# Kernel optimization log

Hardware: AMD Instinct MI355X
Metric: run time of the kernel (lower is better)

## Reference

```python
import jax, jax.numpy as jnp
import numpy as np
import math

B, N, L, ED, H = 2, 32, 4, 64, 4   # graphs, nodes/graph, layers, embed_dim, heads
HD = ED // H
EPS = 1e-5


def _ln(x, g, b):
    m = x.mean(-1, keepdims=True)
    v = ((x - m) ** 2).mean(-1, keepdims=True)
    return (x - m) * jax.lax.rsqrt(v + EPS) * g + b


def _layer(x, W, b, lg, lb, fW, fb, fg, fbeta):
    # NOTE: in the torch source, ModuleList([Linear]*4) shares ONE linear for
    # q/k/v1/v2 and ONE LayerNorm for norms[0..2]; we reproduce that sharing.
    h = (x @ W.T + b).reshape(B, N, N, H, HD)
    q = _ln(h, lg, lb)                                    # q == k (shared LN)
    scores = jnp.einsum('bxahd,bayhd->bxayh', q, q) / math.sqrt(HD)
    att = jax.nn.softmax(scores, axis=2)                  # softmax over 'a'
    xu = jnp.einsum('bxahd,bayhd->bxayhd', h, h)          # v1 == v2 == h
    xu = _ln(xu, lg, lb)                                  # shared LN again
    xu = jnp.einsum('bxayh,bxayhd->bxyhd', att, xu).reshape(B, N, N, ED)
    y = jnp.concatenate([x, xu], axis=-1) @ fW.T + fb
    return _ln(y, fg, fbeta)


def _diag_offdiag_maxpool(x):
    # x: (B, ED, N, N)
    diag = jnp.diagonal(x, axis1=-2, axis2=-1)            # (B, ED, N)
    max_diag = diag.max(axis=2)                           # (B, ED)
    val = jnp.abs(max_diag.max() + (-x).max())
    eye = jnp.eye(N, dtype=x.dtype)
    max_offdiag = (x - val * eye).max(axis=(2, 3))        # (B, ED)
    return jnp.concatenate([max_diag, max_offdiag], axis=1)  # (B, 2*ED)


def setup_inputs() -> dict:
    key = jax.random.key(0)
    ks = jax.random.split(key, 12)
    E = 1024
    g = jax.random.randint(ks[0], (E,), 0, B)
    ls = jax.random.randint(ks[1], (E,), 0, N)
    ld = jax.random.randint(ks[2], (E,), 0, N)
    edge_index = jnp.stack([g * N + ls, g * N + ld]).astype(jnp.int64)
    batch = (jnp.arange(B * N) // N).astype(jnp.int64)
    std = 0.02
    return {
        'edge_index': edge_index,
        'batch': batch,
        'W0': jax.random.normal(ks[3], (ED, 1), jnp.float32) * std,
        'b0': jnp.zeros((ED,), jnp.float32),
        'Ws': jax.random.normal(ks[4], (L - 1, ED, ED), jnp.float32) * std,
        'bs': jnp.zeros((L - 1, ED), jnp.float32),
        'ln_g': jnp.ones((L, HD), jnp.float32),
        'ln_b': jnp.zeros((L, HD), jnp.float32),
        'fW0': jax.random.normal(ks[5], (ED, 1 + ED), jnp.float32) * std,
        'fb0': jnp.zeros((ED,), jnp.float32),
        'fWs': jax.random.normal(ks[6], (L - 1, ED, 2 * ED), jnp.float32) * std,
        'fbs': jnp.zeros((L - 1, ED), jnp.float32),
        'fln_g': jnp.ones((L, ED), jnp.float32),
        'fln_b': jnp.zeros((L, ED), jnp.float32),
        'opW': jax.random.normal(ks[7], (L, ED // 2, 2 * ED), jnp.float32) * std,
        'opb': jnp.zeros((L, ED // 2), jnp.float32),
    }


def reference(edge_index, batch, W0, b0, Ws, bs, ln_g, ln_b,
              fW0, fb0, fWs, fbs, fln_g, fln_b, opW, opb):
    # to_dense_adj with edge_attr = 1.0
    g = batch[edge_index[0]]
    ls = edge_index[0] - g * N
    ld = edge_index[1] - g * N
    adj = jnp.zeros((B, N, N), jnp.float32).at[g, ls, ld].add(1.0)
    idx = jnp.arange(N)
    adj = adj.at[:, idx, idx].set(2.0)
    x = adj[..., None]                                    # (B, N, N, 1)

    scores = jnp.zeros((B, ED // 2), jnp.float32)
    for i in range(L):
        W = W0 if i == 0 else Ws[i - 1]
        b = b0 if i == 0 else bs[i - 1]
        fW = fW0 if i == 0 else fWs[i - 1]
        fb = fb0 if i == 0 else fbs[i - 1]
        x = _layer(x, W, b, ln_g[i], ln_b[i], fW, fb, fln_g[i], fln_b[i])
        pooled = _diag_offdiag_maxpool(jnp.transpose(x, (0, 3, 1, 2)))
        scores = scores + pooled @ opW[i].T + opb[i]

    # BatchNorm1d(momentum=1.0, affine=False), training mode -> batch stats
    m = scores.mean(axis=0)
    v = scores.var(axis=0)
    return (scores - m) / jnp.sqrt(v + EPS)
```

## Files before the change

### kernel.cpp

```cpp
#include <hip/hip_runtime.h>
#include <math.h>

#define EPS 1e-5f

#define AG_LOAD(p)     __hip_atomic_load((p), __ATOMIC_RELAXED, __HIP_MEMORY_SCOPE_AGENT)
#define AG_STORE(p, v) __hip_atomic_store((p), (v), __ATOMIC_RELAXED, __HIP_MEMORY_SCOPE_AGENT)

struct Params {
    const int* ei; const int* batch; int E;
    const float* W0; const float* b0; const float* Ws; const float* bs;
    const float* ln_g; const float* ln_b;
    const float* fW0; const float* fb0; const float* fWs; const float* fbs;
    const float* fln_g; const float* fln_b;
    const float* opW; const float* opb;
    float* hA; float* qA;
    float* hB; float* qB;
    float* xbuf;
    float* Pmin; float* Poff; float* Pdg;
    int* bar;
    float* out;
};

__launch_bounds__(512, 1)
__global__ void k0(Params p) {
    const int tid  = threadIdx.x;
    const int blk  = blockIdx.x;
    const int gtid = blk * 512 + tid;
    const int c    = gtid & 63;
    const int d    = c & 15;
    const int rl   = tid >> 6;
    const int row  = gtid >> 6;
    const int y    = row & 31;
    const int r0     = blk * 8;
    const int b_blk  = r0 >> 10;
    const int xi_blk = (r0 >> 5) & 31;
    const int y0     = r0 & 31;
    const int rld    = xi_blk - y0;

    __shared__ float xslab[32];
    __shared__ float yslab[256];
    __shared__ float xu_s[8][64];
    __shared__ float xrow[8][64];

    if (blk == 0 && tid == 0) p.bar[0] = 0;

    if (tid < 32)  xslab[tid] = 0.0f;
    if (tid < 256) yslab[tid] = 0.0f;
    __syncthreads();
    for (int e2 = tid; e2 < p.E; e2 += 512) {
        int e0 = p.ei[e2], e1 = p.ei[p.E + e2];
        int g  = p.batch[e0];
        if (g == b_blk) {
            int ls = e0 - g * 32, ld = e1 - g * 32;
            if (ls == xi_blk) atomicAdd(&xslab[ld], 1.0f);
            unsigned dy = (unsigned)(ld - y0);
            if (dy < 8u) atomicAdd(&yslab[ls * 8 + dy], 1.0f);
        }
    }
    __syncthreads();
    if (tid == 0) xslab[xi_blk] = 2.0f;
    if (tid < 8)  yslab[(y0 + tid) * 8 + tid] = 2.0f;
    __syncthreads();

    {
        const float gl = p.ln_g[d], bl = p.ln_b[d];
        float Wc = p.W0[c], bc = p.b0[c];
        float sW = Wc, sB = bc;
        #pragma unroll
        for (int m = 1; m < 16; m <<= 1) {
            sW += __shfl_xor(sW, m, 16);
            sB += __shfl_xor(sB, m, 16);
        }
        float Ac = Wc - sW * 0.0625f;
        float Bc = bc - sB * 0.0625f;
        float sAA = Ac * Ac, sAB = Ac * Bc, sBB = Bc * Bc;
        #pragma unroll
        for (int m = 1; m < 16; m <<= 1) {
            sAA += __shfl_xor(sAA, m, 16);
            sAB += __shfl_xor(sAB, m, 16);
            sBB += __shfl_xor(sBB, m, 16);
        }
        const float varW = sAA * 0.0625f, covWB = sAB * 0.0625f, varB = sBB * 0.0625f;
        const float adjv = xslab[y];

        float sarr[32], narr[32];
        #pragma unroll
        for (int a = 0; a < 32; ++a) {
            float vx = xslab[a];
            float vy = yslab[a * 8 + rl];
            float hx = fmaf(Wc, vx, bc);
            float hy = fmaf(Wc, vy, bc);
            float qx = fmaf(Ac, vx, Bc) *
                       rsqrtf(fmaf(fmaf(varW, vx, 2.0f * covWB), vx, varB) + EPS) * gl + bl;
            float qy = fmaf(Ac, vy, Bc) *
                       rsqrtf(fmaf(fmaf(varW, vy, 2.0f * covWB), vy, varB) + EPS) * gl + bl;
            float rdot = qx * qy;
            float pp   = hx * hy;
            float rsum = pp, rsq = pp * pp;
            #pragma unroll
            for (int m = 1; m < 16; m <<= 1) {
                rdot += __shfl_xor(rdot, m, 16);
                rsum += __shfl_xor(rsum, m, 16);
                rsq  += __shfl_xor(rsq,  m, 16);
            }
            sarr[a] = rdot * 0.25f;
            float pmean = rsum * 0.0625f;
            float pvar  = fmaxf(rsq * 0.0625f - pmean * pmean, 0.0f);
            narr[a] = (pp - pmean) * rsqrtf(pvar + EPS) * gl;
        }
        float mx = sarr[0];
        #pragma unroll
        for (int a = 1; a < 32; ++a) mx = fmaxf(mx, sarr[a]);
        float lsum = 0.0f, asum = 0.0f;
        #pragma unroll
        for (int a = 0; a < 32; ++a) {
            float ee = __expf(sarr[a] - mx);
            lsum += ee;
            asum = fmaf(ee, narr[a], asum);
        }
        xu_s[rl][c] = asum / lsum + bl;

        const float* Wr2 = p.fW0 + c * 65;
        float acc2 = fmaf(Wr2[0], adjv, p.fb0[c]);
        #pragma unroll
        for (int j = 0; j < 64; ++j) acc2 = fmaf(Wr2[1 + j], xu_s[rl][j], acc2);
        float t1 = acc2;
        #pragma unroll
        for (int m = 1; m < 64; m <<= 1) t1 += __shfl_xor(t1, m, 64);
        float mu = t1 * (1.0f / 64.0f);
        float dv2 = acc2 - mu;
        float t2 = dv2 * dv2;
        #pragma unroll
        for (int m = 1; m < 64; m <<= 1) t2 += __shfl_xor(t2, m, 64);
        float xnew = dv2 * rsqrtf(t2 * (1.0f / 64.0f) + EPS) * p.fln_g[c] + p.fln_b[c];
        xrow[rl][c]  = xnew;
        p.xbuf[gtid] = xnew;
    }
    __syncthreads();

    if (tid < 64) {
        float mn = 1e30f, off = -1e30f, dg = -1e30f;
        #pragma unroll
        for (int r2 = 0; r2 < 8; ++r2) {
            float v = xrow[r2][tid];
            mn = fminf(mn, v);
            if (r2 == rld) dg = v; else off = fmaxf(off, v);
        }
        int o = blk * 64 + tid;
        p.Pmin[o] = mn; p.Poff[o] = off; p.Pdg[o] = dg;
    }

    {
        const float* Wr = p.Ws + c * 64;
        float acc = p.bs[c];
        #pragma unroll
        for (int j = 0; j < 64; ++j) acc = fmaf(Wr[j], xrow[rl][j], acc);
        p.hA[gtid] = acc;
        float s1 = acc;
        #pragma unroll
        for (int m = 1; m < 16; m <<= 1) s1 += __shfl_xor(s1, m, 16);
        float mean = s1 * 0.0625f;
        float dv = acc - mean;
        float s2 = dv * dv;
        #pragma unroll
        for (int m = 1; m < 16; m <<= 1) s2 += __shfl_xor(s2, m, 16);
        p.qA[gtid] = dv * rsqrtf(s2 * 0.0625f + EPS) * p.ln_g[16 + d] + p.ln_b[16 + d];
    }
}

__launch_bounds__(512, 1)
__global__ void klayer(Params p, int layer, int is_last) {
    const int tid  = threadIdx.x;
    const int blk  = blockIdx.x;
    const int gtid = blk * 512 + tid;
    const int c    = gtid & 63;
    const int d    = c & 15;
    const int rl   = tid >> 6;
    const int row  = gtid >> 6;
    const int y    = row & 31;
    const int b    = row >> 10;
    const int r0     = blk * 8;
    const int b_blk  = r0 >> 10;
    const int xi_blk = (r0 >> 5) & 31;
    const int y0     = r0 & 31;
    const int rld    = xi_blk - y0;
    const int slab_off = (b_blk * 1024 + xi_blk * 32) * 64;

    const float* hin = (layer == 2) ? p.hB : p.hA;
    const float* qin = (layer == 2) ? p.qB : p.qA;
    float* hout = (layer == 1) ? p.hB : p.hA;
    float* qout = (layer == 1) ? p.qB : p.qA;

    __shared__ float qx_s[2048], hx_s[2048];
    __shared__ float xrow[8][64], xu_s[8][64];
    __shared__ float sm_mn[512], sm_off[512], sm_dg[512];
    __shared__ float psum[512];
    __shared__ float vals[4];
    __shared__ float scores_s[64];
    __shared__ int tailflag;

    float xv = p.xbuf[gtid];
    float4 qsl = ((const float4*)(qin + slab_off))[tid];
    float4 hsl = ((const float4*)(hin + slab_off))[tid];
    const float* qy = qin + (b * 1024 + y) * 64 + c;
    const float* hy = hin + (b * 1024 + y) * 64 + c;
    float qyv[32], hyv[32];
    #pragma unroll
    for (int a = 0; a < 32; ++a) {
        qyv[a] = qy[a * 2048];
        hyv[a] = hy[a * 2048];
    }
    xrow[rl][c] = xv;
    ((float4*)qx_s)[tid] = qsl;
    ((float4*)hx_s)[tid] = hsl;
    __syncthreads();

    const float gl = p.ln_g[layer * 16 + d], bl = p.ln_b[layer * 16 + d];
    float sarr[32], narr[32];
    #pragma unroll
    for (int a = 0; a < 32; ++a) {
        float qxv = qx_s[a * 64 + c];
        float hxv = hx_s[a * 64 + c];
        float rdot = qxv * qyv[a];
        float pp   = hxv * hyv[a];
        float rsum = pp, rsq = pp * pp;
        #pragma unroll
        for (int m = 1; m < 16; m <<= 1) {
            rdot += __shfl_xor(rdot, m, 16);
            rsum += __shfl_xor(rsum, m, 16);
            rsq  += __shfl_xor(rsq,  m, 16);
        }
        sarr[a] = rdot * 0.25f;
        float pmean = rsum * 0.0625f;
        float pvar  = fmaxf(rsq * 0.0625f - pmean * pmean, 0.0f);
        narr[a] = (pp - pmean) * rsqrtf(pvar + EPS) * gl;
    }
    float mx = sarr[0];
    #pragma unroll
    for (int a = 1; a < 32; ++a) mx = fmaxf(mx, sarr[a]);
    float lsum = 0.0f, asum = 0.0f;
    #pragma unroll
    for (int a = 0; a < 32; ++a) {
        float ee = __expf(sarr[a] - mx);
        lsum += ee;
        asum = fmaf(ee, narr[a], asum);
    }
    xu_s[rl][c] = asum / lsum + bl;

    const float* Wr2 = p.fWs + (layer - 1) * 8192 + c * 128;
    float acc2 = p.fbs[(layer - 1) * 64 + c];
    #pragma unroll
    for (int j = 0; j < 64; ++j) acc2 = fmaf(Wr2[j], xrow[rl][j], acc2);
    #pragma unroll
    for (int j = 0; j < 64; ++j) acc2 = fmaf(Wr2[64 + j], xu_s[rl][j], acc2);
    float t1 = acc2;
    #pragma unroll
    for (int m = 1; m < 64; m <<= 1) t1 += __shfl_xor(t1, m, 64);
    float mu = t1 * (1.0f / 64.0f);
    float dv2 = acc2 - mu;
    float t2 = dv2 * dv2;
    #pragma unroll
    for (int m = 1; m < 64; m <<= 1) t2 += __shfl_xor(t2, m, 64);
    float xnew = dv2 * rsqrtf(t2 * (1.0f / 64.0f) + EPS) *
                 p.fln_g[layer * 64 + c] + p.fln_b[layer * 64 + c];
    __syncthreads();
    xrow[rl][c] = xnew;
    if (!is_last) p.xbuf[gtid] = xnew;
    __syncthreads();

    if (tid < 64) {
        float mn = 1e30f, off = -1e30f, dg = -1e30f;
        #pragma unroll
        for (int r2 = 0; r2 < 8; ++r2) {
            float v = xrow[r2][tid];
            mn = fminf(mn, v);
            if (r2 == rld) dg = v; else off = fmaxf(off, v);
        }
        int o = layer * 16384 + blk * 64 + tid;
        if (is_last) {
            AG_STORE(&p.Pmin[o], mn); AG_STORE(&p.Poff[o], off); AG_STORE(&p.Pdg[o], dg);
        } else {
            p.Pmin[o] = mn; p.Poff[o] = off; p.Pdg[o] = dg;
        }
    }

    if (!is_last) {
        const float* Wr = p.Ws + layer * 4096 + c * 64;
        float acc = p.bs[layer * 64 + c];
        #pragma unroll
        for (int j = 0; j < 64; ++j) acc = fmaf(Wr[j], xrow[rl][j], acc);
        hout[gtid] = acc;
        float s1 = acc;
        #pragma unroll
        for (int m = 1; m < 16; m <<= 1) s1 += __shfl_xor(s1, m, 16);
        float mean = s1 * 0.0625f;
        float dv = acc - mean;
        float s2 = dv * dv;
        #pragma unroll
        for (int m = 1; m < 16; m <<= 1) s2 += __shfl_xor(s2, m, 16);
        qout[gtid] = dv * rsqrtf(s2 * 0.0625f + EPS) *
                     p.ln_g[(layer + 1) * 16 + d] + p.ln_b[(layer + 1) * 16 + d];
        return;
    }

    __syncthreads();
    if (tid == 0) {
        int r = __hip_atomic_fetch_add(p.bar, 1, __ATOMIC_RELAXED,
                                       __HIP_MEMORY_SCOPE_AGENT);
        tailflag = (r == 255) ? 1 : 0;
    }
    __syncthreads();
    if (!tailflag) return;

    {
        int l = tid >> 7, bb = (tid >> 6) & 1, e = tid & 63;
        float mn = 1e30f, off = -1e30f, dg = -1e30f;
        for (int k = 0; k < 128; ++k) {
            int o = l * 16384 + (bb * 128 + k) * 64 + e;
            float vmn, voff, vdg;
            if (l == 3) { vmn = AG_LOAD(&p.Pmin[o]); voff = AG_LOAD(&p.Poff[o]); vdg = AG_LOAD(&p.Pdg[o]); }
            else        { vmn = p.Pmin[o];           voff = p.Poff[o];           vdg = p.Pdg[o]; }
            mn  = fminf(mn,  vmn);
            off = fmaxf(off, voff);
            dg  = fmaxf(dg,  vdg);
        }
        sm_mn[tid] = mn; sm_off[tid] = off; sm_dg[tid] = dg;
    }
    __syncthreads();
    if (tid < 4) {
        float gmx = -1e30f, gmn = 1e30f;
        for (int i2 = 0; i2 < 128; ++i2) {
            gmx = fmaxf(gmx, sm_dg[tid * 128 + i2]);
            gmn = fminf(gmn, sm_mn[tid * 128 + i2]);
        }
        vals[tid] = fabsf(gmx - gmn);
    }
    __syncthreads();
    {
        int bb = tid >> 8, cc = (tid >> 3) & 31, pp = tid & 7;
        float a2 = 0.0f;
        for (int l = 0; l < 4; ++l) {
            float val = vals[l];
            const float* Wr = p.opW + l * 4096 + cc * 128;
            int base = l * 128 + bb * 64;
            for (int j = pp * 16; j < pp * 16 + 16; ++j) {
                float pv;
                if (j < 64) pv = sm_dg[base + j];
                else        pv = fmaxf(sm_off[base + j - 64], sm_dg[base + j - 64] - val);
                a2 = fmaf(Wr[j], pv, a2);
            }
        }
        psum[tid] = a2;
    }
    __syncthreads();
    if (tid < 64) {
        int bb = tid >> 5, cc = tid & 31;
        float a2 = 0.0f;
        for (int l = 0; l < 4; ++l) a2 += p.opb[l * 32 + cc];
        for (int pp = 0; pp < 8; ++pp) a2 += psum[bb * 256 + cc * 8 + pp];
        scores_s[tid] = a2;
    }
    __syncthreads();
    if (tid < 32) {
        float sA = scores_s[tid], sB = scores_s[32 + tid];
        float mu2 = 0.5f * (sA + sB);
        float va = 0.5f * ((sA - mu2) * (sA - mu2) + (sB - mu2) * (sB - mu2));
        float inv = rsqrtf(va + EPS);
        p.out[tid]      = (sA - mu2) * inv;
        p.out[32 + tid] = (sB - mu2) * inv;
    }
}

extern "C" void kernel_launch(void* const* d_in, const int* in_sizes, int n_in,
                              void* d_out, int out_size, void* d_ws, size_t ws_size,
                              hipStream_t stream) {
    Params prm;
    prm.ei    = (const int*)d_in[0];
    prm.batch = (const int*)d_in[1];
    prm.E     = in_sizes[0] / 2;
    prm.W0    = (const float*)d_in[2];
    prm.b0    = (const float*)d_in[3];
    prm.Ws    = (const float*)d_in[4];
    prm.bs    = (const float*)d_in[5];
    prm.ln_g  = (const float*)d_in[6];
    prm.ln_b  = (const float*)d_in[7];
    prm.fW0   = (const float*)d_in[8];
    prm.fb0   = (const float*)d_in[9];
    prm.fWs   = (const float*)d_in[10];
    prm.fbs   = (const float*)d_in[11];
    prm.fln_g = (const float*)d_in[12];
    prm.fln_b = (const float*)d_in[13];
    prm.opW   = (const float*)d_in[14];
    prm.opb   = (const float*)d_in[15];

    float* ws = (float*)d_ws;
    prm.hA    = ws;
    prm.qA    = prm.hA   + 131072;
    prm.hB    = prm.qA   + 131072;
    prm.qB    = prm.hB   + 131072;
    prm.xbuf  = prm.qB   + 131072;
    prm.Pmin  = prm.xbuf + 131072;
    prm.Poff  = prm.Pmin + 65536;
    prm.Pdg   = prm.Poff + 65536;
    prm.bar   = (int*)(prm.Pdg + 65536);
    prm.out   = (float*)d_out;

    k0<<<256, 512, 0, stream>>>(prm);
    klayer<<<256, 512, 0, stream>>>(prm, 1, 0);
    klayer<<<256, 512, 0, stream>>>(prm, 2, 0);
    klayer<<<256, 512, 0, stream>>>(prm, 3, 1);
}
```

Measured before the change: 196.7 us.

## Use online softmax and chunked y-loads to cut register pressure in layer kernels

```diff
diff --git a/kernel.cpp b/kernel.cpp
--- a/kernel.cpp
+++ b/kernel.cpp
@@ -39,14 +39,15 @@
 
     __shared__ float xslab[32];
     __shared__ float yslab[256];
-    __shared__ float xu_s[8][64];
-    __shared__ float xrow[8][64];
+    __shared__ float xu[512];
+    __shared__ float xrow[512];
 
     if (blk == 0 && tid == 0) p.bar[0] = 0;
 
     if (tid < 32)  xslab[tid] = 0.0f;
     if (tid < 256) yslab[tid] = 0.0f;
     __syncthreads();
+    #pragma unroll 1
     for (int e2 = tid; e2 < p.E; e2 += 512) {
         int e0 = p.ei[e2], e1 = p.ei[p.E + e2];
         int g  = p.batch[e0];
@@ -62,87 +63,84 @@
     if (tid < 8)  yslab[(y0 + tid) * 8 + tid] = 2.0f;
     __syncthreads();
 
+    const float gl = p.ln_g[d], bl = p.ln_b[d];
+    float Wc = p.W0[c], bc = p.b0[c];
+    float sW = Wc, sB = bc;
+    #pragma unroll
+    for (int m = 1; m < 16; m <<= 1) {
+        sW += __shfl_xor(sW, m, 16);
+        sB += __shfl_xor(sB, m, 16);
+    }
+    float Ac = Wc - sW * 0.0625f;
+    float Bc = bc - sB * 0.0625f;
+    float sAA = Ac * Ac, sAB = Ac * Bc, sBB = Bc * Bc;
+    #pragma unroll
+    for (int m = 1; m < 16; m <<= 1) {
+        sAA += __shfl_xor(sAA, m, 16);
+        sAB += __shfl_xor(sAB, m, 16);
+        sBB += __shfl_xor(sBB, m, 16);
+    }
+    const float varW = sAA * 0.0625f, covWB = sAB * 0.0625f, varB = sBB * 0.0625f;
+    const float adjv = xslab[y];
+
+    float mrun = -1e30f, lrun = 0.0f, arun = 0.0f;
+    #pragma unroll 1
+    for (int a = 0; a < 32; ++a) {
+        float vx = xslab[a];
+        float vy = yslab[a * 8 + rl];
+        float hx = fmaf(Wc, vx, bc);
+        float hy = fmaf(Wc, vy, bc);
+        float qx = fmaf(Ac, vx, Bc) *
+                   rsqrtf(fmaf(fmaf(varW, vx, 2.0f * covWB), vx, varB) + EPS) * gl + bl;
+        float qy = fmaf(Ac, vy, Bc) *
+                   rsqrtf(fmaf(fmaf(varW, vy, 2.0f * covWB), vy, varB) + EPS) * gl + bl;
+        float rdot = qx * qy;
+        float pp   = hx * hy;
+        float rsum = pp, rsq = pp * pp;
+        #pragma unroll
+        for (int m = 1; m < 16; m <<= 1) {
+            rdot += __shfl_xor(rdot, m, 16);
+            rsum += __shfl_xor(rsum, m, 16);
+            rsq  += __shfl_xor(rsq,  m, 16);
+        }
+        float s     = rdot * 0.25f;
+        float pmean = rsum * 0.0625f;
+        float pvar  = fmaxf(rsq * 0.0625f - pmean * pmean, 0.0f);
+        float nrm   = (pp - pmean) * rsqrtf(pvar + EPS) * gl;
+        float nm  = fmaxf(mrun, s);
+        float scl = __expf(mrun - nm);
+        float e   = __expf(s - nm);
+        lrun = lrun * scl + e;
+        arun = arun * scl + e * nrm;
+        mrun = nm;
+    }
+    xu[tid] = arun / lrun + bl;
+
+    const float* Wr2 = p.fW0 + c * 65;
+    float acc2 = fmaf(Wr2[0], adjv, p.fb0[c]);
     {
-        const float gl = p.ln_g[d], bl = p.ln_b[d];
-        float Wc = p.W0[c], bc = p.b0[c];
-        float sW = Wc, sB = bc;
-        #pragma unroll
-        for (int m = 1; m < 16; m <<= 1) {
-            sW += __shfl_xor(sW, m, 16);
-            sB += __shfl_xor(sB, m, 16);
-        }
-        float Ac = Wc - sW * 0.0625f;
-        float Bc = bc - sB * 0.0625f;
-        float sAA = Ac * Ac, sAB = Ac * Bc, sBB = Bc * Bc;
-        #pragma unroll
-        for (int m = 1; m < 16; m <<= 1) {
-            sAA += __shfl_xor(sAA, m, 16);
-            sAB += __shfl_xor(sAB, m, 16);
-            sBB += __shfl_xor(sBB, m, 16);
-        }
-        const float varW = sAA * 0.0625f, covWB = sAB * 0.0625f, varB = sBB * 0.0625f;
-        const float adjv = xslab[y];
-
-        float sarr[32], narr[32];
-        #pragma unroll
-        for (int a = 0; a < 32; ++a) {
-            float vx = xslab[a];
-            float vy = yslab[a * 8 + rl];
-            float hx = fmaf(Wc, vx, bc);
-            float hy = fmaf(Wc, vy, bc);
-            float qx = fmaf(Ac, vx, Bc) *
-                       rsqrtf(fmaf(fmaf(varW, vx, 2.0f * covWB), vx, varB) + EPS) * gl + bl;
-            float qy = fmaf(Ac, vy, Bc) *
-                       rsqrtf(fmaf(fmaf(varW, vy, 2.0f * covWB), vy, varB) + EPS) * gl + bl;
-            float rdot = qx * qy;
-            float pp   = hx * hy;
-            float rsum = pp, rsq = pp * pp;
-            #pragma unroll
-            for (int m = 1; m < 16; m <<= 1) {
-                rdot += __shfl_xor(rdot, m, 16);
-                rsum += __shfl_xor(rsum, m, 16);
-                rsq  += __shfl_xor(rsq,  m, 16);
-            }
-            sarr[a] = rdot * 0.25f;
-            float pmean = rsum * 0.0625f;
-            float pvar  = fmaxf(rsq * 0.0625f - pmean * pmean, 0.0f);
-            narr[a] = (pp - pmean) * rsqrtf(pvar + EPS) * gl;
-        }
-        float mx = sarr[0];
-        #pragma unroll
-        for (int a = 1; a < 32; ++a) mx = fmaxf(mx, sarr[a]);
-        float lsum = 0.0f, asum = 0.0f;
-        #pragma unroll
-        for (int a = 0; a < 32; ++a) {
-            float ee = __expf(sarr[a] - mx);
-            lsum += ee;
-            asum = fmaf(ee, narr[a], asum);
-        }
-        xu_s[rl][c] = asum / lsum + bl;
-
-        const float* Wr2 = p.fW0 + c * 65;
-        float acc2 = fmaf(Wr2[0], adjv, p.fb0[c]);
-        #pragma unroll
-        for (int j = 0; j < 64; ++j) acc2 = fmaf(Wr2[1 + j], xu_s[rl][j], acc2);
-        float t1 = acc2;
-        #pragma unroll
-        for (int m = 1; m < 64; m <<= 1) t1 += __shfl_xor(t1, m, 64);
-        float mu = t1 * (1.0f / 64.0f);
-        float dv2 = acc2 - mu;
-        float t2 = dv2 * dv2;
-        #pragma unroll
-        for (int m = 1; m < 64; m <<= 1) t2 += __shfl_xor(t2, m, 64);
-        float xnew = dv2 * rsqrtf(t2 * (1.0f / 64.0f) + EPS) * p.fln_g[c] + p.fln_b[c];
-        xrow[rl][c]  = xnew;
-        p.xbuf[gtid] = xnew;
-    }
+        const float* xw = xu + rl * 64;
+        #pragma unroll 8
+        for (int j = 0; j < 64; ++j) acc2 = fmaf(Wr2[1 + j], xw[j], acc2);
+    }
+    float t1 = acc2;
+    #pragma unroll
+    for (int m = 1; m < 64; m <<= 1) t1 += __shfl_xor(t1, m, 64);
+    float mu = t1 * (1.0f / 64.0f);
+    float dv2 = acc2 - mu;
+    float t2 = dv2 * dv2;
+    #pragma unroll
+    for (int m = 1; m < 64; m <<= 1) t2 += __shfl_xor(t2, m, 64);
+    float xnew = dv2 * rsqrtf(t2 * (1.0f / 64.0f) + EPS) * p.fln_g[c] + p.fln_b[c];
+    xrow[tid]    = xnew;
+    p.xbuf[gtid] = xnew;
     __syncthreads();
 
     if (tid < 64) {
         float mn = 1e30f, off = -1e30f, dg = -1e30f;
         #pragma unroll
         for (int r2 = 0; r2 < 8; ++r2) {
-            float v = xrow[r2][tid];
+            float v = xrow[r2 * 64 + tid];
             mn = fminf(mn, v);
             if (r2 == rld) dg = v; else off = fmaxf(off, v);
         }
@@ -151,10 +149,14 @@
     }
 
     {
-        const float* Wr = p.Ws + c * 64;
+        const float4* W4 = (const float4*)(p.Ws + c * 64);
+        const float4* X4 = (const float4*)(xrow + rl * 64);
         float acc = p.bs[c];
-        #pragma unroll
-        for (int j = 0; j < 64; ++j) acc = fmaf(Wr[j], xrow[rl][j], acc);
+        #pragma unroll 4
+        for (int j = 0; j < 16; ++j) {
+            float4 w = W4[j], x = X4[j];
+            acc += w.x * x.x + w.y * x.y + w.z * x.z + w.w * x.w;
+        }
         p.hA[gtid] = acc;
         float s1 = acc;
         #pragma unroll
@@ -192,7 +194,7 @@
     float* qout = (layer == 1) ? p.qB : p.qA;
 
     __shared__ float qx_s[2048], hx_s[2048];
-    __shared__ float xrow[8][64], xu_s[8][64];
+    __shared__ float xrow[512], xu[512];
     __shared__ float sm_mn[512], sm_off[512], sm_dg[512];
     __shared__ float psum[512];
     __shared__ float vals[4];
@@ -200,59 +202,71 @@
     __shared__ int tailflag;
 
     float xv = p.xbuf[gtid];
-    float4 qsl = ((const float4*)(qin + slab_off))[tid];
-    float4 hsl = ((const float4*)(hin + slab_off))[tid];
+    float4 qs = ((const float4*)(qin + slab_off))[tid];
+    float4 hs = ((const float4*)(hin + slab_off))[tid];
+    xrow[tid] = xv;
+    ((float4*)qx_s)[tid] = qs;
+    ((float4*)hx_s)[tid] = hs;
+    __syncthreads();
+
+    const float gl = p.ln_g[layer * 16 + d], bl = p.ln_b[layer * 16 + d];
     const float* qy = qin + (b * 1024 + y) * 64 + c;
     const float* hy = hin + (b * 1024 + y) * 64 + c;
-    float qyv[32], hyv[32];
-    #pragma unroll
-    for (int a = 0; a < 32; ++a) {
-        qyv[a] = qy[a * 2048];
-        hyv[a] = hy[a * 2048];
-    }
-    xrow[rl][c] = xv;
-    ((float4*)qx_s)[tid] = qsl;
-    ((float4*)hx_s)[tid] = hsl;
-    __syncthreads();
-
-    const float gl = p.ln_g[layer * 16 + d], bl = p.ln_b[layer * 16 + d];
-    float sarr[32], narr[32];
-    #pragma unroll
-    for (int a = 0; a < 32; ++a) {
-        float qxv = qx_s[a * 64 + c];
-        float hxv = hx_s[a * 64 + c];
-        float rdot = qxv * qyv[a];
-        float pp   = hxv * hyv[a];
-        float rsum = pp, rsq = pp * pp;
-        #pragma unroll
-        for (int m = 1; m < 16; m <<= 1) {
-            rdot += __shfl_xor(rdot, m, 16);
-            rsum += __shfl_xor(rsum, m, 16);
-            rsq  += __shfl_xor(rsq,  m, 16);
-        }
-        sarr[a] = rdot * 0.25f;
-        float pmean = rsum * 0.0625f;
-        float pvar  = fmaxf(rsq * 0.0625f - pmean * pmean, 0.0f);
-        narr[a] = (pp - pmean) * rsqrtf(pvar + EPS) * gl;
-    }
-    float mx = sarr[0];
-    #pragma unroll
-    for (int a = 1; a < 32; ++a) mx = fmaxf(mx, sarr[a]);
-    float lsum = 0.0f, asum = 0.0f;
-    #pragma unroll
-    for (int a = 0; a < 32; ++a) {
-        float ee = __expf(sarr[a] - mx);
-        lsum += ee;
-        asum = fmaf(ee, narr[a], asum);
-    }
-    xu_s[rl][c] = asum / lsum + bl;
-
-    const float* Wr2 = p.fWs + (layer - 1) * 8192 + c * 128;
+
+    float mrun = -1e30f, lrun = 0.0f, arun = 0.0f;
+    #pragma unroll 1
+    for (int ch = 0; ch < 4; ++ch) {
+        float qv8[8], hv8[8];
+        const float* qpc = qy + ch * 8 * 2048;
+        const float* hpc = hy + ch * 8 * 2048;
+        #pragma unroll
+        for (int k = 0; k < 8; ++k) {
+            qv8[k] = qpc[k * 2048];
+            hv8[k] = hpc[k * 2048];
+        }
+        const float* qxc = qx_s + ch * 8 * 64 + c;
+        const float* hxc = hx_s + ch * 8 * 64 + c;
+        #pragma unroll
+        for (int k = 0; k < 8; ++k) {
+            float rdot = qxc[k * 64] * qv8[k];
+            float pp   = hxc[k * 64] * hv8[k];
+            float rsum = pp, rsq = pp * pp;
+            #pragma unroll
+            for (int m = 1; m < 16; m <<= 1) {
+                rdot += __shfl_xor(rdot, m, 16);
+                rsum += __shfl_xor(rsum, m, 16);
+                rsq  += __shfl_xor(rsq,  m, 16);
+            }
+            float s     = rdot * 0.25f;
+            float pmean = rsum * 0.0625f;
+            float pvar  = fmaxf(rsq * 0.0625f - pmean * pmean, 0.0f);
+            float nrm   = (pp - pmean) * rsqrtf(pvar + EPS) * gl;
+            float nm  = fmaxf(mrun, s);
+            float scl = __expf(mrun - nm);
+            float e   = __expf(s - nm);
+            lrun = lrun * scl + e;
+            arun = arun * scl + e * nrm;
+            mrun = nm;
+        }
+    }
+    xu[tid] = arun / lrun + bl;
+
     float acc2 = p.fbs[(layer - 1) * 64 + c];
-    #pragma unroll
-    for (int j = 0; j < 64; ++j) acc2 = fmaf(Wr2[j], xrow[rl][j], acc2);
-    #pragma unroll
-    for (int j = 0; j < 64; ++j) acc2 = fmaf(Wr2[64 + j], xu_s[rl][j], acc2);
+    {
+        const float4* W4 = (const float4*)(p.fWs + (layer - 1) * 8192 + c * 128);
+        const float4* Xa = (const float4*)(xrow + rl * 64);
+        const float4* Xb = (const float4*)(xu + rl * 64);
+        #pragma unroll 4
+        for (int j = 0; j < 16; ++j) {
+            float4 w = W4[j], x = Xa[j];
+            acc2 += w.x * x.x + w.y * x.y + w.z * x.z + w.w * x.w;
+        }
+        #pragma unroll 4
+        for (int j = 0; j < 16; ++j) {
+            float4 w = W4[16 + j], x = Xb[j];
+            acc2 += w.x * x.x + w.y * x.y + w.z * x.z + w.w * x.w;
+        }
+    }
     float t1 = acc2;
     #pragma unroll
     for (int m = 1; m < 64; m <<= 1) t1 += __shfl_xor(t1, m, 64);
@@ -263,8 +277,7 @@
     for (int m = 1; m < 64; m <<= 1) t2 += __shfl_xor(t2, m, 64);
     float xnew = dv2 * rsqrtf(t2 * (1.0f / 64.0f) + EPS) *
                  p.fln_g[layer * 64 + c] + p.fln_b[layer * 64 + c];
-    __syncthreads();
-    xrow[rl][c] = xnew;
+    xrow[tid] = xnew;
     if (!is_last) p.xbuf[gtid] = xnew;
     __syncthreads();
 
@@ -272,7 +285,7 @@
         float mn = 1e30f, off = -1e30f, dg = -1e30f;
         #pragma unroll
         for (int r2 = 0; r2 < 8; ++r2) {
-            float v = xrow[r2][tid];
+            float v = xrow[r2 * 64 + tid];
             mn = fminf(mn, v);
             if (r2 == rld) dg = v; else off = fmaxf(off, v);
         }
@@ -285,10 +298,14 @@
     }
 
     if (!is_last) {
-        const float* Wr = p.Ws + layer * 4096 + c * 64;
+        const float4* W4 = (const float4*)(p.Ws + layer * 4096 + c * 64);
+        const float4* X4 = (const float4*)(xrow + rl * 64);
         float acc = p.bs[layer * 64 + c];
-        #pragma unroll
-        for (int j = 0; j < 64; ++j) acc = fmaf(Wr[j], xrow[rl][j], acc);
+        #pragma unroll 4
+        for (int j = 0; j < 16; ++j) {
+            float4 w = W4[j], x = X4[j];
+            acc += w.x * x.x + w.y * x.y + w.z * x.z + w.w * x.w;
+        }
         hout[gtid] = acc;
         float s1 = acc;
         #pragma unroll
@@ -303,7 +320,6 @@
         return;
     }
 
-    __syncthreads();
     if (tid == 0) {
         int r = __hip_atomic_fetch_add(p.bar, 1, __ATOMIC_RELAXED,
                                        __HIP_MEMORY_SCOPE_AGENT);
@@ -315,20 +331,30 @@
     {
         int l = tid >> 7, bb = (tid >> 6) & 1, e = tid & 63;
         float mn = 1e30f, off = -1e30f, dg = -1e30f;
-        for (int k = 0; k < 128; ++k) {
-            int o = l * 16384 + (bb * 128 + k) * 64 + e;
-            float vmn, voff, vdg;
-            if (l == 3) { vmn = AG_LOAD(&p.Pmin[o]); voff = AG_LOAD(&p.Poff[o]); vdg = AG_LOAD(&p.Pdg[o]); }
-            else        { vmn = p.Pmin[o];           voff = p.Poff[o];           vdg = p.Pdg[o]; }
-            mn  = fminf(mn,  vmn);
-            off = fmaxf(off, voff);
-            dg  = fmaxf(dg,  vdg);
+        int base = l * 16384 + bb * 128 * 64 + e;
+        if (l == 3) {
+            #pragma unroll 4
+            for (int k = 0; k < 128; ++k) {
+                int o = base + k * 64;
+                mn  = fminf(mn,  AG_LOAD(&p.Pmin[o]));
+                off = fmaxf(off, AG_LOAD(&p.Poff[o]));
+                dg  = fmaxf(dg,  AG_LOAD(&p.Pdg[o]));
+            }
+        } else {
+            #pragma unroll 4
+            for (int k = 0; k < 128; ++k) {
+                int o = base + k * 64;
+                mn  = fminf(mn,  p.Pmin[o]);
+                off = fmaxf(off, p.Poff[o]);
+                dg  = fmaxf(dg,  p.Pdg[o]);
+            }
         }
         sm_mn[tid] = mn; sm_off[tid] = off; sm_dg[tid] = dg;
     }
     __syncthreads();
     if (tid < 4) {
         float gmx = -1e30f, gmn = 1e30f;
+        #pragma unroll 1
         for (int i2 = 0; i2 < 128; ++i2) {
             gmx = fmaxf(gmx, sm_dg[tid * 128 + i2]);
             gmn = fminf(gmn, sm_mn[tid * 128 + i2]);
@@ -339,10 +365,12 @@
     {
         int bb = tid >> 8, cc = (tid >> 3) & 31, pp = tid & 7;
         float a2 = 0.0f;
+        #pragma unroll 1
         for (int l = 0; l < 4; ++l) {
             float val = vals[l];
             const float* Wr = p.opW + l * 4096 + cc * 128;
             int base = l * 128 + bb * 64;
+            #pragma unroll 1
             for (int j = pp * 16; j < pp * 16 + 16; ++j) {
                 float pv;
                 if (j < 64) pv = sm_dg[base + j];
@@ -356,7 +384,9 @@
     if (tid < 64) {
         int bb = tid >> 5, cc = tid & 31;
         float a2 = 0.0f;
+        #pragma unroll
         for (int l = 0; l < 4; ++l) a2 += p.opb[l * 32 + cc];
+        #pragma unroll
         for (int pp = 0; pp < 8; ++pp) a2 += psum[bb * 256 + cc * 8 + pp];
         scores_s[tid] = a2;
     }
```

Result: slower. 203.8 us (+3.7%).

## Split attention reduction across two waves per row with online-softmax merge

Applied to the files above, without the earlier changes.

```diff
diff --git a/kernel.cpp b/kernel.cpp
--- a/kernel.cpp
+++ b/kernel.cpp
@@ -47,6 +47,7 @@
     if (tid < 32)  xslab[tid] = 0.0f;
     if (tid < 256) yslab[tid] = 0.0f;
     __syncthreads();
+    #pragma unroll 1
     for (int e2 = tid; e2 < p.E; e2 += 512) {
         int e0 = p.ei[e2], e1 = p.ei[p.E + e2];
         int g  = p.batch[e0];
@@ -62,80 +63,78 @@
     if (tid < 8)  yslab[(y0 + tid) * 8 + tid] = 2.0f;
     __syncthreads();
 
-    {
-        const float gl = p.ln_g[d], bl = p.ln_b[d];
-        float Wc = p.W0[c], bc = p.b0[c];
-        float sW = Wc, sB = bc;
+    const float gl = p.ln_g[d], bl = p.ln_b[d];
+    float Wc = p.W0[c], bc = p.b0[c];
+    float sW = Wc, sB = bc;
+    #pragma unroll
+    for (int m = 1; m < 16; m <<= 1) {
+        sW += __shfl_xor(sW, m, 16);
+        sB += __shfl_xor(sB, m, 16);
+    }
+    float Ac = Wc - sW * 0.0625f;
+    float Bc = bc - sB * 0.0625f;
+    float sAA = Ac * Ac, sAB = Ac * Bc, sBB = Bc * Bc;
+    #pragma unroll
+    for (int m = 1; m < 16; m <<= 1) {
+        sAA += __shfl_xor(sAA, m, 16);
+        sAB += __shfl_xor(sAB, m, 16);
+        sBB += __shfl_xor(sBB, m, 16);
+    }
+    const float varW = sAA * 0.0625f, covWB = sAB * 0.0625f, varB = sBB * 0.0625f;
+    const float adjv = xslab[y];
+
+    float sarr[32], narr[32];
+    #pragma unroll
+    for (int a = 0; a < 32; ++a) {
+        float vx = xslab[a];
+        float vy = yslab[a * 8 + rl];
+        float hx = fmaf(Wc, vx, bc);
+        float hy = fmaf(Wc, vy, bc);
+        float qx = fmaf(Ac, vx, Bc) *
+                   rsqrtf(fmaf(fmaf(varW, vx, 2.0f * covWB), vx, varB) + EPS) * gl + bl;
+        float qy = fmaf(Ac, vy, Bc) *
+                   rsqrtf(fmaf(fmaf(varW, vy, 2.0f * covWB), vy, varB) + EPS) * gl + bl;
+        float rdot = qx * qy;
+        float pp   = hx * hy;
+        float rsum = pp, rsq = pp * pp;
         #pragma unroll
         for (int m = 1; m < 16; m <<= 1) {
-            sW += __shfl_xor(sW, m, 16);
-            sB += __shfl_xor(sB, m, 16);
-        }
-        float Ac = Wc - sW * 0.0625f;
-        float Bc = bc - sB * 0.0625f;
-        float sAA = Ac * Ac, sAB = Ac * Bc, sBB = Bc * Bc;
-        #pragma unroll
-        for (int m = 1; m < 16; m <<= 1) {
-            sAA += __shfl_xor(sAA, m, 16);
-            sAB += __shfl_xor(sAB, m, 16);
-            sBB += __shfl_xor(sBB, m, 16);
-        }
-        const float varW = sAA * 0.0625f, covWB = sAB * 0.0625f, varB = sBB * 0.0625f;
-        const float adjv = xslab[y];
-
-        float sarr[32], narr[32];
-        #pragma unroll
-        for (int a = 0; a < 32; ++a) {
-            float vx = xslab[a];
-            float vy = yslab[a * 8 + rl];
-            float hx = fmaf(Wc, vx, bc);
-            float hy = fmaf(Wc, vy, bc);
-            float qx = fmaf(Ac, vx, Bc) *
-                       rsqrtf(fmaf(fmaf(varW, vx, 2.0f * covWB), vx, varB) + EPS) * gl + bl;
-            float qy = fmaf(Ac, vy, Bc) *
-                       rsqrtf(fmaf(fmaf(varW, vy, 2.0f * covWB), vy, varB) + EPS) * gl + bl;
-            float rdot = qx * qy;
-            float pp   = hx * hy;
-            float rsum = pp, rsq = pp * pp;
-            #pragma unroll
-            for (int m = 1; m < 16; m <<= 1) {
-                rdot += __shfl_xor(rdot, m, 16);
-                rsum += __shfl_xor(rsum, m, 16);
-                rsq  += __shfl_xor(rsq,  m, 16);
-            }
-            sarr[a] = rdot * 0.25f;
-            float pmean = rsum * 0.0625f;
-            float pvar  = fmaxf(rsq * 0.0625f - pmean * pmean, 0.0f);
-            narr[a] = (pp - pmean) * rsqrtf(pvar + EPS) * gl;
-        }
-        float mx = sarr[0];
-        #pragma unroll
-        for (int a = 1; a < 32; ++a) mx = fmaxf(mx, sarr[a]);
-        float lsum = 0.0f, asum = 0.0f;
-        #pragma unroll
-        for (int a = 0; a < 32; ++a) {
-            float ee = __expf(sarr[a] - mx);
-            lsum += ee;
-            asum = fmaf(ee, narr[a], asum);
-        }
-        xu_s[rl][c] = asum / lsum + bl;
-
-        const float* Wr2 = p.fW0 + c * 65;
-        float acc2 = fmaf(Wr2[0], adjv, p.fb0[c]);
-        #pragma unroll
-        for (int j = 0; j < 64; ++j) acc2 = fmaf(Wr2[1 + j], xu_s[rl][j], acc2);
-        float t1 = acc2;
-        #pragma unroll
-        for (int m = 1; m < 64; m <<= 1) t1 += __shfl_xor(t1, m, 64);
-        float mu = t1 * (1.0f / 64.0f);
-        float dv2 = acc2 - mu;
-        float t2 = dv2 * dv2;
-        #pragma unroll
-        for (int m = 1; m < 64; m <<= 1) t2 += __shfl_xor(t2, m, 64);
-        float xnew = dv2 * rsqrtf(t2 * (1.0f / 64.0f) + EPS) * p.fln_g[c] + p.fln_b[c];
-        xrow[rl][c]  = xnew;
-        p.xbuf[gtid] = xnew;
-    }
+            rdot += __shfl_xor(rdot, m, 16);
+            rsum += __shfl_xor(rsum, m, 16);
+            rsq  += __shfl_xor(rsq,  m, 16);
+        }
+        sarr[a] = rdot * 0.25f;
+        float pmean = rsum * 0.0625f;
+        float pvar  = fmaxf(rsq * 0.0625f - pmean * pmean, 0.0f);
+        narr[a] = (pp - pmean) * rsqrtf(pvar + EPS) * gl;
+    }
+    float mx = sarr[0];
+    #pragma unroll
+    for (int a = 1; a < 32; ++a) mx = fmaxf(mx, sarr[a]);
+    float lsum = 0.0f, asum = 0.0f;
+    #pragma unroll
+    for (int a = 0; a < 32; ++a) {
+        float ee = __expf(sarr[a] - mx);
+        lsum += ee;
+        asum = fmaf(ee, narr[a], asum);
+    }
+    xu_s[rl][c] = asum / lsum + bl;
+
+    const float* Wr2 = p.fW0 + c * 65;
+    float acc2 = fmaf(Wr2[0], adjv, p.fb0[c]);
+    #pragma unroll
+    for (int j = 0; j < 64; ++j) acc2 = fmaf(Wr2[1 + j], xu_s[rl][j], acc2);
+    float t1 = acc2;
+    #pragma unroll
+    for (int m = 1; m < 64; m <<= 1) t1 += __shfl_xor(t1, m, 64);
+    float mu = t1 * (1.0f / 64.0f);
+    float dv2 = acc2 - mu;
+    float t2 = dv2 * dv2;
+    #pragma unroll
+    for (int m = 1; m < 64; m <<= 1) t2 += __shfl_xor(t2, m, 64);
+    float xnew = dv2 * rsqrtf(t2 * (1.0f / 64.0f) + EPS) * p.fln_g[c] + p.fln_b[c];
+    xrow[rl][c]  = xnew;
+    p.xbuf[gtid] = xnew;
     __syncthreads();
 
     if (tid < 64) {
@@ -168,17 +167,19 @@
     }
 }
 
-__launch_bounds__(512, 1)
+__launch_bounds__(1024, 1)
 __global__ void klayer(Params p, int layer, int is_last) {
     const int tid  = threadIdx.x;
     const int blk  = blockIdx.x;
-    const int gtid = blk * 512 + tid;
-    const int c    = gtid & 63;
+    const int rl   = tid >> 7;
+    const int u    = tid & 127;
+    const int w    = u >> 6;
+    const int c    = u & 63;
     const int d    = c & 15;
-    const int rl   = tid >> 6;
-    const int row  = gtid >> 6;
+    const int row  = blk * 8 + rl;
     const int y    = row & 31;
     const int b    = row >> 10;
+    const int ge   = row * 64 + c;
     const int r0     = blk * 8;
     const int b_blk  = r0 >> 10;
     const int xi_blk = (r0 >> 5) & 31;
@@ -192,37 +193,37 @@
     float* qout = (layer == 1) ? p.qB : p.qA;
 
     __shared__ float qx_s[2048], hx_s[2048];
-    __shared__ float xrow[8][64], xu_s[8][64];
+    __shared__ float xrow[512], xu[512];
+    __shared__ float mM[1024], mL[1024], mA[1024];
     __shared__ float sm_mn[512], sm_off[512], sm_dg[512];
     __shared__ float psum[512];
     __shared__ float vals[4];
     __shared__ float scores_s[64];
     __shared__ int tailflag;
 
-    float xv = p.xbuf[gtid];
-    float4 qsl = ((const float4*)(qin + slab_off))[tid];
-    float4 hsl = ((const float4*)(hin + slab_off))[tid];
+    if (w == 0) xrow[rl * 64 + c] = p.xbuf[ge];
+    ((float2*)qx_s)[tid] = ((const float2*)(qin + slab_off))[tid];
+    ((float2*)hx_s)[tid] = ((const float2*)(hin + slab_off))[tid];
     const float* qy = qin + (b * 1024 + y) * 64 + c;
     const float* hy = hin + (b * 1024 + y) * 64 + c;
-    float qyv[32], hyv[32];
-    #pragma unroll
-    for (int a = 0; a < 32; ++a) {
-        qyv[a] = qy[a * 2048];
-        hyv[a] = hy[a * 2048];
-    }
-    xrow[rl][c] = xv;
-    ((float4*)qx_s)[tid] = qsl;
-    ((float4*)hx_s)[tid] = hsl;
+    float qyv[16], hyv[16];
+    #pragma unroll
+    for (int k = 0; k < 16; ++k) {
+        qyv[k] = qy[(w * 16 + k) * 2048];
+        hyv[k] = hy[(w * 16 + k) * 2048];
+    }
     __syncthreads();
 
     const float gl = p.ln_g[layer * 16 + d], bl = p.ln_b[layer * 16 + d];
-    float sarr[32], narr[32];
-    #pragma unroll
-    for (int a = 0; a < 32; ++a) {
+
+    float sarr[16], narr[16];
+    #pragma unroll
+    for (int k = 0; k < 16; ++k) {
+        int a = w * 16 + k;
         float qxv = qx_s[a * 64 + c];
         float hxv = hx_s[a * 64 + c];
-        float rdot = qxv * qyv[a];
-        float pp   = hxv * hyv[a];
+        float rdot = qxv * qyv[k];
+        float pp   = hxv * hyv[k];
         float rsum = pp, rsq = pp * pp;
         #pragma unroll
         for (int m = 1; m < 16; m <<= 1) {
@@ -230,49 +231,63 @@
             rsum += __shfl_xor(rsum, m, 16);
             rsq  += __shfl_xor(rsq,  m, 16);
         }
-        sarr[a] = rdot * 0.25f;
+        sarr[k] = rdot * 0.25f;
         float pmean = rsum * 0.0625f;
         float pvar  = fmaxf(rsq * 0.0625f - pmean * pmean, 0.0f);
-        narr[a] = (pp - pmean) * rsqrtf(pvar + EPS) * gl;
+        narr[k] = (pp - pmean) * rsqrtf(pvar + EPS) * gl;
     }
     float mx = sarr[0];
     #pragma unroll
-    for (int a = 1; a < 32; ++a) mx = fmaxf(mx, sarr[a]);
+    for (int k = 1; k < 16; ++k) mx = fmaxf(mx, sarr[k]);
     float lsum = 0.0f, asum = 0.0f;
     #pragma unroll
-    for (int a = 0; a < 32; ++a) {
-        float ee = __expf(sarr[a] - mx);
+    for (int k = 0; k < 16; ++k) {
+        float ee = __expf(sarr[k] - mx);
         lsum += ee;
-        asum = fmaf(ee, narr[a], asum);
-    }
-    xu_s[rl][c] = asum / lsum + bl;
-
-    const float* Wr2 = p.fWs + (layer - 1) * 8192 + c * 128;
-    float acc2 = p.fbs[(layer - 1) * 64 + c];
-    #pragma unroll
-    for (int j = 0; j < 64; ++j) acc2 = fmaf(Wr2[j], xrow[rl][j], acc2);
-    #pragma unroll
-    for (int j = 0; j < 64; ++j) acc2 = fmaf(Wr2[64 + j], xu_s[rl][j], acc2);
-    float t1 = acc2;
-    #pragma unroll
-    for (int m = 1; m < 64; m <<= 1) t1 += __shfl_xor(t1, m, 64);
-    float mu = t1 * (1.0f / 64.0f);
-    float dv2 = acc2 - mu;
-    float t2 = dv2 * dv2;
-    #pragma unroll
-    for (int m = 1; m < 64; m <<= 1) t2 += __shfl_xor(t2, m, 64);
-    float xnew = dv2 * rsqrtf(t2 * (1.0f / 64.0f) + EPS) *
-                 p.fln_g[layer * 64 + c] + p.fln_b[layer * 64 + c];
-    __syncthreads();
-    xrow[rl][c] = xnew;
-    if (!is_last) p.xbuf[gtid] = xnew;
+        asum = fmaf(ee, narr[k], asum);
+    }
+    const int mi = w * 512 + rl * 64 + c;
+    mM[mi] = mx; mL[mi] = lsum; mA[mi] = asum;
+    __syncthreads();
+
+    float xnew = 0.0f;
+    if (w == 0) {
+        const int mo = 512 + rl * 64 + c;
+        float m1 = mM[mo], l1 = mL[mo], a1 = mA[mo];
+        float mm = fmaxf(mx, m1);
+        float e0 = __expf(mx - mm), e1 = __expf(m1 - mm);
+        float lt = lsum * e0 + l1 * e1;
+        float at = asum * e0 + a1 * e1;
+        xu[rl * 64 + c] = at / lt + bl;
+
+        const float* Wr2 = p.fWs + (layer - 1) * 8192 + c * 128;
+        float acc2 = p.fbs[(layer - 1) * 64 + c];
+        const float* xa = xrow + rl * 64;
+        const float* xb = xu + rl * 64;
+        #pragma unroll
+        for (int j = 0; j < 64; ++j) acc2 = fmaf(Wr2[j], xa[j], acc2);
+        #pragma unroll
+        for (int j = 0; j < 64; ++j) acc2 = fmaf(Wr2[64 + j], xb[j], acc2);
+        float t1 = acc2;
+        #pragma unroll
+        for (int m = 1; m < 64; m <<= 1) t1 += __shfl_xor(t1, m, 64);
+        float mu = t1 * (1.0f / 64.0f);
+        float dv2 = acc2 - mu;
+        float t2 = dv2 * dv2;
+        #pragma unroll
+        for (int m = 1; m < 64; m <<= 1) t2 += __shfl_xor(t2, m, 64);
+        xnew = dv2 * rsqrtf(t2 * (1.0f / 64.0f) + EPS) *
+               p.fln_g[layer * 64 + c] + p.fln_b[layer * 64 + c];
+        xrow[rl * 64 + c] = xnew;
+        if (!is_last) p.xbuf[ge] = xnew;
+    }
     __syncthreads();
 
     if (tid < 64) {
         float mn = 1e30f, off = -1e30f, dg = -1e30f;
         #pragma unroll
         for (int r2 = 0; r2 < 8; ++r2) {
-            float v = xrow[r2][tid];
+            float v = xrow[r2 * 64 + tid];
             mn = fminf(mn, v);
             if (r2 == rld) dg = v; else off = fmaxf(off, v);
         }
@@ -285,25 +300,27 @@
     }
 
     if (!is_last) {
-        const float* Wr = p.Ws + layer * 4096 + c * 64;
-        float acc = p.bs[layer * 64 + c];
-        #pragma unroll
-        for (int j = 0; j < 64; ++j) acc = fmaf(Wr[j], xrow[rl][j], acc);
-        hout[gtid] = acc;
-        float s1 = acc;
-        #pragma unroll
-        for (int m = 1; m < 16; m <<= 1) s1 += __shfl_xor(s1, m, 16);
-        float mean = s1 * 0.0625f;
-        float dv = acc - mean;
-        float s2 = dv * dv;
-        #pragma unroll
-        for (int m = 1; m < 16; m <<= 1) s2 += __shfl_xor(s2, m, 16);
-        qout[gtid] = dv * rsqrtf(s2 * 0.0625f + EPS) *
-                     p.ln_g[(layer + 1) * 16 + d] + p.ln_b[(layer + 1) * 16 + d];
+        if (w == 0) {
+            const float* Wr = p.Ws + layer * 4096 + c * 64;
+            const float* xa = xrow + rl * 64;
+            float acc = p.bs[layer * 64 + c];
+            #pragma unroll
+            for (int j = 0; j < 64; ++j) acc = fmaf(Wr[j], xa[j], acc);
+            hout[ge] = acc;
+            float s1 = acc;
+            #pragma unroll
+            for (int m = 1; m < 16; m <<= 1) s1 += __shfl_xor(s1, m, 16);
+            float mean = s1 * 0.0625f;
+            float dv = acc - mean;
+            float s2 = dv * dv;
+            #pragma unroll
+            for (int m = 1; m < 16; m <<= 1) s2 += __shfl_xor(s2, m, 16);
+            qout[ge] = dv * rsqrtf(s2 * 0.0625f + EPS) *
+                       p.ln_g[(layer + 1) * 16 + d] + p.ln_b[(layer + 1) * 16 + d];
+        }
         return;
     }
 
-    __syncthreads();
     if (tid == 0) {
         int r = __hip_atomic_fetch_add(p.bar, 1, __ATOMIC_RELAXED,
                                        __HIP_MEMORY_SCOPE_AGENT);
@@ -312,23 +329,33 @@
     __syncthreads();
     if (!tailflag) return;
 
-    {
+    if (tid < 512) {
         int l = tid >> 7, bb = (tid >> 6) & 1, e = tid & 63;
         float mn = 1e30f, off = -1e30f, dg = -1e30f;
-        for (int k = 0; k < 128; ++k) {
-            int o = l * 16384 + (bb * 128 + k) * 64 + e;
-            float vmn, voff, vdg;
-            if (l == 3) { vmn = AG_LOAD(&p.Pmin[o]); voff = AG_LOAD(&p.Poff[o]); vdg = AG_LOAD(&p.Pdg[o]); }
-            else        { vmn = p.Pmin[o];           voff = p.Poff[o];           vdg = p.Pdg[o]; }
-            mn  = fminf(mn,  vmn);
-            off = fmaxf(off, voff);
-            dg  = fmaxf(dg,  vdg);
+        int base = l * 16384 + bb * 128 * 64 + e;
+        if (l == 3) {
+            #pragma unroll 4
+            for (int k = 0; k < 128; ++k) {
+                int o = base + k * 64;
+                mn  = fminf(mn,  AG_LOAD(&p.Pmin[o]));
+                off = fmaxf(off, AG_LOAD(&p.Poff[o]));
+                dg  = fmaxf(dg,  AG_LOAD(&p.Pdg[o]));
+            }
+        } else {
+            #pragma unroll 4
+            for (int k = 0; k < 128; ++k) {
+                int o = base + k * 64;
+                mn  = fminf(mn,  p.Pmin[o]);
+                off = fmaxf(off, p.Poff[o]);
+                dg  = fmaxf(dg,  p.Pdg[o]);
+            }
         }
         sm_mn[tid] = mn; sm_off[tid] = off; sm_dg[tid] = dg;
     }
     __syncthreads();
     if (tid < 4) {
         float gmx = -1e30f, gmn = 1e30f;
+        #pragma unroll 1
         for (int i2 = 0; i2 < 128; ++i2) {
             gmx = fmaxf(gmx, sm_dg[tid * 128 + i2]);
             gmn = fminf(gmn, sm_mn[tid * 128 + i2]);
@@ -336,13 +363,15 @@
         vals[tid] = fabsf(gmx - gmn);
     }
     __syncthreads();
-    {
+    if (tid < 512) {
         int bb = tid >> 8, cc = (tid >> 3) & 31, pp = tid & 7;
         float a2 = 0.0f;
+        #pragma unroll 1
         for (int l = 0; l < 4; ++l) {
             float val = vals[l];
             const float* Wr = p.opW + l * 4096 + cc * 128;
             int base = l * 128 + bb * 64;
+            #pragma unroll 1
             for (int j = pp * 16; j < pp * 16 + 16; ++j) {
                 float pv;
                 if (j < 64) pv = sm_dg[base + j];
@@ -356,7 +385,9 @@
     if (tid < 64) {
         int bb = tid >> 5, cc = tid & 31;
         float a2 = 0.0f;
+        #pragma unroll
         for (int l = 0; l < 4; ++l) a2 += p.opb[l * 32 + cc];
+        #pragma unroll
         for (int pp = 0; pp < 8; ++pp) a2 += psum[bb * 256 + cc * 8 + pp];
         scores_s[tid] = a2;
     }
@@ -406,7 +437,7 @@
     prm.out   = (float*)d_out;
 
     k0<<<256, 512, 0, stream>>>(prm);
-    klayer<<<256, 512, 0, stream>>>(prm, 1, 0);
-    klayer<<<256, 512, 0, stream>>>(prm, 2, 0);
-    klayer<<<256, 512, 0, stream>>>(prm, 3, 1);
+    klayer<<<256, 1024, 0, stream>>>(prm, 1, 0);
+    klayer<<<256, 1024, 0, stream>>>(prm, 2, 0);
+    klayer<<<256, 1024, 0, stream>>>(prm, 3, 1);
 }
```

After: 212.1 us. 1.08x slower.
